# Optimization experiments

Measured on AMD Instinct MI355X. Metric: run time of the kernel, lower is better.

## Reference

```python
import itertools
import jax, jax.numpy as jnp
import numpy as np

# static block configuration
B, C, H, W, DIM, HEADS = 2, 4, 60, 120, 512, 8
WS = (2, 6, 12)          # window size (Wc, Wh, Ww)
SS = (1, 3, 6)           # shift size
N = WS[0] * WS[1] * WS[2]            # 144 tokens per window
C1, H1, W1 = C // WS[0], H // WS[1], W // WS[2]
NW = C1 * H1 * W1                    # windows per sample
DH = DIM // HEADS
EPS = 1e-6


def _attn_bias():
    """Static shifted-window attention bias (nW, N, N): 0 within group, -inf across.
    Mirrors compute_3d_shifted_window_mask (warped=True, longitude wrap merge)."""
    img = np.zeros((C, H, W), np.int32)
    c_sl = ((0, C - WS[0]), (C - WS[0], C - SS[0]), (C - SS[0], C))
    h_sl = ((0, H - WS[1]), (H - WS[1], H - SS[1]), (H - SS[1], H))
    w_sl = ((0, W - WS[2]), (W - WS[2], W - SS[2]), (W - SS[2], W))
    cnt = 0
    for (cs, ce), (hs, he), (ws_, we) in itertools.product(c_sl, h_sl, w_sl):
        img[cs:ce, hs:he, ws_:we] = cnt
        cnt += 1
    # warped (periodic longitude) group merges
    for i in range(3):
        for a, b in ((1, 2), (4, 5), (7, 8)):
            img[img == a + 9 * i] = b + 9 * i
    m = img.reshape(C1, WS[0], H1, WS[1], W1, WS[2])
    m = m.transpose(0, 2, 4, 1, 3, 5).reshape(NW, N)
    diff = m[:, None, :] - m[:, :, None]
    return jnp.asarray(np.where(diff != 0, -np.inf, 0.0).astype(np.float32))


_BIAS = _attn_bias()[None, :, None, :, :]  # (1, nW, 1, N, N)


def _ln(x, s, b):
    mu = x.mean(-1, keepdims=True)
    var = x.var(-1, keepdims=True)
    return (x - mu) / jnp.sqrt(var + EPS) * s + b


def setup_inputs() -> dict:
    key = jax.random.key(0)
    ks = jax.random.split(key, 6)
    s = 0.02
    return {
        "x": jax.random.normal(ks[0], (B, C * H * W, DIM), jnp.float32),
        "qkv_w": jax.random.normal(ks[1], (DIM, 3 * DIM), jnp.float32) * s,
        "qkv_b": jnp.zeros((3 * DIM,), jnp.float32),
        "proj_w": jax.random.normal(ks[2], (DIM, DIM), jnp.float32) * s,
        "proj_b": jnp.zeros((DIM,), jnp.float32),
        "norm1_scale": jnp.ones((DIM,), jnp.float32),
        "norm1_bias": jnp.zeros((DIM,), jnp.float32),
        "norm2_scale": jnp.ones((DIM,), jnp.float32),
        "norm2_bias": jnp.zeros((DIM,), jnp.float32),
        "mlp_w1": jax.random.normal(ks[3], (DIM, 4 * DIM), jnp.float32) * s,
        "mlp_b1": jnp.zeros((4 * DIM,), jnp.float32),
        "mlp_w2": jax.random.normal(ks[4], (4 * DIM, DIM), jnp.float32) * s,
        "mlp_b2": jnp.zeros((DIM,), jnp.float32),
    }


def reference(x, qkv_w, qkv_b, proj_w, proj_b, norm1_scale, norm1_bias,
              norm2_scale, norm2_bias, mlp_w1, mlp_b1, mlp_w2, mlp_b2):
    shortcut = x                                   # (B, L, D)
    h = _ln(x, norm1_scale, norm1_bias).reshape(B, C, H, W, DIM)
    # cyclic shift
    h = jnp.roll(h, (-SS[0], -SS[1], -SS[2]), axis=(1, 2, 3))
    # window partition: (B,C,H,W,D) -> (B*nW, N, D)
    h = h.reshape(B, C1, WS[0], H1, WS[1], W1, WS[2], DIM)
    h = h.transpose(0, 1, 3, 5, 2, 4, 6, 7).reshape(B * NW, N, DIM)
    # windowed multi-head self-attention
    qkv = h @ qkv_w + qkv_b                        # (B*nW, N, 3*D)
    qkv = qkv.reshape(B, NW, N, 3, HEADS, DH)
    q = qkv[..., 0, :, :].transpose(0, 1, 3, 2, 4)  # (B, nW, H, N, Dh)
    k = qkv[..., 1, :, :].transpose(0, 1, 3, 2, 4)
    v = qkv[..., 2, :, :].transpose(0, 1, 3, 2, 4)
    scale = 1.0 / float(np.sqrt(DH))
    attn = jnp.einsum("bwhnd,bwhmd->bwhnm", q, k) * scale + _BIAS
    attn = jax.nn.softmax(attn, axis=-1)
    o = jnp.einsum("bwhnm,bwhmd->bwhnd", attn, v)
    o = o.transpose(0, 1, 3, 2, 4).reshape(B * NW, N, DIM)
    o = o @ proj_w + proj_b
    # window reverse: (B*nW, N, D) -> (B,C,H,W,D)
    o = o.reshape(B, C1, H1, W1, WS[0], WS[1], WS[2], DIM)
    o = o.transpose(0, 1, 4, 2, 5, 3, 6, 7).reshape(B, C, H, W, DIM)
    # reverse cyclic shift
    o = jnp.roll(o, SS, axis=(1, 2, 3))
    x = shortcut + o.reshape(B, C * H * W, DIM)    # drop_path is identity
    # MLP block
    h2 = _ln(x, norm2_scale, norm2_bias)
    h2 = jax.nn.gelu(h2 @ mlp_w1 + mlp_b1) @ mlp_w2 + mlp_b2
    return x + h2
```

## Files before the change

kernel.cpp:

```cpp
#include <hip/hip_runtime.h>

typedef __attribute__((ext_vector_type(8))) short bf16x8;
typedef __attribute__((ext_vector_type(4))) float f32x4;
typedef __attribute__((ext_vector_type(8))) unsigned short u16x8;

#define BAR() __builtin_amdgcn_s_barrier()
#define VMC(n) asm volatile("s_waitcnt vmcnt(" #n ")" ::: "memory")
#define SB0() __builtin_amdgcn_sched_barrier(0)
#define WAITL() do { asm volatile("s_waitcnt lgkmcnt(0)"); SB0(); } while (0)
#define DSRI(dst, base, imm) \
  asm volatile("ds_read_b128 %0, %1 offset:%2" : "=&v"(dst) : "v"(base), "i"(imm))

__device__ inline unsigned short f2bf(float f) {
  unsigned int u = __float_as_uint(f);
  u += 0x7fffu + ((u >> 16) & 1u);
  return (unsigned short)(u >> 16);
}

__device__ inline void gload_lds16(const void* g, void* l) {
  __builtin_amdgcn_global_load_lds(
      (const __attribute__((address_space(1))) void*)g,
      (__attribute__((address_space(3))) void*)l, 16, 0, 0);
}

__global__ void wtrans(const float* __restrict__ W, unsigned short* __restrict__ Wt,
                       int K, int N) {
  int idx = blockIdx.x * 256 + threadIdx.x;
  if (idx >= K * N) return;
  int k = idx / N, n = idx - k * N;
  Wt[(size_t)n * K + k] = f2bf(W[idx]);
}

template <int MODE>
__global__ void ln_k(const float* __restrict__ x, const float* __restrict__ sc,
                     const float* __restrict__ bi, unsigned short* __restrict__ o) {
  int t = blockIdx.x * 4 + (threadIdx.x >> 6);
  int l = threadIdx.x & 63;
  size_t src;
  if (MODE == 0) {
    int b = t / 28800, r = t - b * 28800;
    int win = r / 144, tok = r - win * 144;
    int c1 = win / 100, rem = win - c1 * 100;
    int h1 = rem / 10, w1 = rem - h1 * 10;
    int tc = tok / 72, tr = tok - tc * 72;
    int th = tr / 12, tw = tr - th * 12;
    int cs = c1 * 2 + tc, hs = h1 * 6 + th, wsp = w1 * 12 + tw;
    int co = (cs + 1) & 3;
    int ho = hs + 3; if (ho >= 60) ho -= 60;
    int wo = wsp + 6; if (wo >= 120) wo -= 120;
    src = ((size_t)b * 28800 + (co * 60 + ho) * 120 + wo) * 512;
  } else {
    src = (size_t)t * 512;
  }
  const float4* xr = (const float4*)(x + src);
  float4 v0 = xr[l * 2], v1 = xr[l * 2 + 1];
  float s = v0.x + v0.y + v0.z + v0.w + v1.x + v1.y + v1.z + v1.w;
  float s2 = v0.x * v0.x + v0.y * v0.y + v0.z * v0.z + v0.w * v0.w +
             v1.x * v1.x + v1.y * v1.y + v1.z * v1.z + v1.w * v1.w;
  #pragma unroll
  for (int o2 = 32; o2; o2 >>= 1) {
    s += __shfl_xor(s, o2);
    s2 += __shfl_xor(s2, o2);
  }
  float mean = s * (1.0f / 512.0f);
  float var = s2 * (1.0f / 512.0f) - mean * mean;
  float inv = rsqrtf(var + 1e-6f);
  const float4* scp = (const float4*)sc;
  const float4* bip = (const float4*)bi;
  float4 sa = scp[l * 2], sb = scp[l * 2 + 1];
  float4 ba = bip[l * 2], bb = bip[l * 2 + 1];
  u16x8 ov;
  ov[0] = f2bf((v0.x - mean) * inv * sa.x + ba.x);
  ov[1] = f2bf((v0.y - mean) * inv * sa.y + ba.y);
  ov[2] = f2bf((v0.z - mean) * inv * sa.z + ba.z);
  ov[3] = f2bf((v0.w - mean) * inv * sa.w + ba.w);
  ov[4] = f2bf((v1.x - mean) * inv * sb.x + bb.x);
  ov[5] = f2bf((v1.y - mean) * inv * sb.y + bb.y);
  ov[6] = f2bf((v1.z - mean) * inv * sb.z + bb.z);
  ov[7] = f2bf((v1.w - mean) * inv * sb.w + bb.w);
  *(u16x8*)&o[(size_t)t * 512 + l * 8] = ov;
}

template <int EPI>
__launch_bounds__(256, 2)
__global__ void gemmT(const unsigned short* __restrict__ A,
                      const unsigned short* __restrict__ Bt,
                      const float* __restrict__ bias, void* __restrict__ outp,
                      const float* __restrict__ res, int M, int N, int K) {
  __shared__ __attribute__((aligned(16))) unsigned short lds3[3][12288];
  const int tid = threadIdx.x;
  const int w = tid >> 6, l = tid & 63;
  const int lane15 = l & 15, lk = (l >> 4) << 3;
  const int ntile = N >> 8;
  const int nwg = gridDim.x;
  const int q = nwg >> 3, r = nwg & 7;
  const int xcd = blockIdx.x & 7, idx8 = blockIdx.x >> 3;
  const int wgid = (xcd < r ? xcd * (q + 1) : r * (q + 1) + (xcd - r) * q) + idx8;
  const int bm = wgid / ntile, bn = wgid - bm * ntile;
  const int KT = K >> 5;

  const int swzb = ((l >> 3) & 3) << 3;
  const int colx = (((l & 3) << 3) ^ swzb);
  const int rA0 = (0 * 4 + w) * 16 + (l >> 2);
  const int rA1 = (1 * 4 + w) * 16 + (l >> 2);
  const int offA0 = (rA0 * K + colx) * 2, offA1 = (rA1 * K + colx) * 2;
  int offB[4];
  #pragma unroll
  for (int j = 0; j < 4; ++j)
    offB[j] = (((j * 4 + w) * 16 + (l >> 2)) * K + colx) * 2;

  const int sw = ((lane15 >> 1) & 3) << 3;
  unsigned lds0 = (unsigned)(unsigned long long)
      (__attribute__((address_space(3))) void*)(void*)&lds3[0][0];
  const unsigned comA = (unsigned)(lane15 * 64 + ((lk ^ sw) << 1));
  unsigned bA0 = lds0 + comA;
  unsigned bA1 = bA0 + 24576u, bA2 = bA0 + 49152u;
  const unsigned bOffB = 8192u + ((unsigned)w << 12);
  unsigned bB0 = bA0 + bOffB, bB1 = bA1 + bOffB, bB2 = bA2 + bOffB;

  unsigned short* p0 = &lds3[0][0];
  unsigned short* p1 = &lds3[1][0];
  unsigned short* p2 = &lds3[2][0];

  const char* gA = (const char*)(A + (size_t)bm * 128 * K);
  const char* gB = (const char*)(Bt + (size_t)bn * 256 * K);

  f32x4 acc[8][4] = {};
  bf16x8 afL[4], afH[4], bfr[4];

  auto STAGE = [&](unsigned short* pS, const char* ga, const char* gb) {
    gload_lds16(ga + offA0, pS + w * 512);
    gload_lds16(ga + offA1, pS + 2048 + w * 512);
    #pragma unroll
    for (int j = 0; j < 4; ++j)
      gload_lds16(gb + offB[j], pS + 4096 + (j * 4 + w) * 512);
  };

  STAGE(p0, gA, gB); gA += 64; gB += 64;
  STAGE(p1, gA, gB); gA += 64; gB += 64;
  VMC(6);
  BAR();

  for (int t = 0; t < KT; ++t) {
    DSRI(afL[0], bA0, 0);    DSRI(afL[1], bA0, 1024);
    DSRI(afL[2], bA0, 2048); DSRI(afL[3], bA0, 3072);
    DSRI(bfr[0], bB0, 0);    DSRI(bfr[1], bB0, 1024);
    DSRI(bfr[2], bB0, 2048); DSRI(bfr[3], bB0, 3072);
    if (t < KT - 2) {
      STAGE(p2, gA, gB);
      gA += 64; gB += 64;
    }
    WAITL();
    DSRI(afH[0], bA0, 4096); DSRI(afH[1], bA0, 5120);
    DSRI(afH[2], bA0, 6144); DSRI(afH[3], bA0, 7168);
    SB0();
    __builtin_amdgcn_s_setprio(1);
    #pragma unroll
    for (int mf = 0; mf < 4; ++mf)
      #pragma unroll
      for (int nf = 0; nf < 4; ++nf)
        acc[mf][nf] = __builtin_amdgcn_mfma_f32_16x16x32_bf16(
            afL[mf], bfr[nf], acc[mf][nf], 0, 0, 0);
    __builtin_amdgcn_s_setprio(0);
    WAITL();
    __builtin_amdgcn_s_setprio(1);
    #pragma unroll
    for (int mf = 0; mf < 4; ++mf)
      #pragma unroll
      for (int nf = 0; nf < 4; ++nf)
        acc[4 + mf][nf] = __builtin_amdgcn_mfma_f32_16x16x32_bf16(
            afH[mf], bfr[nf], acc[4 + mf][nf], 0, 0, 0);
    __builtin_amdgcn_s_setprio(0);
    if (t < KT - 2) { VMC(6); } else if (t == KT - 2) { VMC(0); }
    if (t < KT - 1) BAR();
    unsigned ta = bA0; bA0 = bA1; bA1 = bA2; bA2 = ta;
    unsigned tb = bB0; bB0 = bB1; bB1 = bB2; bB2 = tb;
    unsigned short* tp = p0; p0 = p1; p1 = p2; p2 = tp;
  }

  float* outf = (float*)outp;
  unsigned short* outh = (unsigned short*)outp;
  #pragma unroll
  for (int mi = 0; mi < 8; ++mi) {
    #pragma unroll
    for (int j = 0; j < 4; ++j) {
      int grow = bm * 128 + mi * 16 + ((l >> 4) << 2) + j;
      int win = 0, tok = 0;
      size_t rowbase = 0;
      if constexpr (EPI == 0) {
        win = grow / 144;
        tok = grow - win * 144;
      } else if constexpr (EPI == 1) {
        win = grow / 144;
        tok = grow - win * 144;
        int b = win / 200, wl = win - b * 200;
        int c1 = wl / 100, rem = wl - c1 * 100;
        int h1 = rem / 10, w1 = rem - h1 * 10;
        int tc = tok / 72, tr = tok - tc * 72;
        int th = tr / 12, tw = tr - th * 12;
        int cs = c1 * 2 + tc, hs = h1 * 6 + th, wsp = w1 * 12 + tw;
        int co = (cs + 1) & 3;
        int ho = hs + 3; if (ho >= 60) ho -= 60;
        int wo = wsp + 6; if (wo >= 120) wo -= 120;
        rowbase = ((size_t)b * 28800 + (co * 60 + ho) * 120 + wo) * 512;
      }
      #pragma unroll
      for (int nf = 0; nf < 4; ++nf) {
        int gcol = bn * 256 + w * 64 + nf * 16 + lane15;
        float val = acc[mi][nf][j] + bias[gcol];
        if constexpr (EPI == 0) {
          int which = gcol >> 9, hd = (gcol >> 6) & 7, dh = gcol & 63;
          outh[(((size_t)(win * 3 + which) * 8 + hd) * 144 + tok) * 64 + dh] = f2bf(val);
        } else if constexpr (EPI == 1) {
          size_t oi = rowbase + gcol;
          outf[oi] = res[oi] + val;
        } else if constexpr (EPI == 2) {
          float u = 0.7978845608f * (val + 0.044715f * val * val * val);
          float g = val / (1.0f + __expf(-2.0f * u));
          outh[(size_t)grow * N + gcol] = f2bf(g);
        } else {
          size_t oi = (size_t)grow * N + gcol;
          outf[oi] += val;
        }
      }
    }
  }
}

__launch_bounds__(576)
__global__ void attn_k(const unsigned short* __restrict__ qkv,
                       unsigned short* __restrict__ owin) {
  __shared__ __attribute__((aligned(16))) unsigned short Ks[144 * 72];
  __shared__ __attribute__((aligned(16))) unsigned short Vt[64 * 168];
  __shared__ __attribute__((aligned(16))) unsigned short Ps[144 * 168];
  __shared__ unsigned char gid[144];
  int bid = blockIdx.x;
  int win = bid >> 3, head = bid & 7;
  const unsigned short* qb = qkv + ((size_t)(win * 3 + 0) * 8 + head) * (144 * 64);
  const unsigned short* kb = qkv + ((size_t)(win * 3 + 1) * 8 + head) * (144 * 64);
  const unsigned short* vb = qkv + ((size_t)(win * 3 + 2) * 8 + head) * (144 * 64);
  int tid = threadIdx.x;
  {
    int row = tid >> 2, c0 = (tid & 3) << 4;
    u16x8 ka = *(const u16x8*)(kb + row * 64 + c0);
    u16x8 kc = *(const u16x8*)(kb + row * 64 + c0 + 8);
    *(u16x8*)&Ks[row * 72 + c0] = ka;
    *(u16x8*)&Ks[row * 72 + c0 + 8] = kc;
    u16x8 va = *(const u16x8*)(vb + row * 64 + c0);
    u16x8 vc = *(const u16x8*)(vb + row * 64 + c0 + 8);
    #pragma unroll
    for (int j = 0; j < 8; ++j) Vt[(c0 + j) * 168 + row] = va[j];
    #pragma unroll
    for (int j = 0; j < 8; ++j) Vt[(c0 + 8 + j) * 168 + row] = vc[j];
  }
  for (int i = tid; i < 64 * 24; i += 576) {
    int d = i / 24, m = i - d * 24;
    Vt[d * 168 + 144 + m] = 0;
  }
  for (int i = tid; i < 144 * 24; i += 576) {
    int r = i / 24, c = i - r * 24;
    Ps[r * 168 + 144 + c] = 0;
  }
  if (tid < 144) {
    int wl = win % 200;
    int c1 = wl / 100, rem = wl - c1 * 100;
    int h1 = rem / 10, w1 = rem - h1 * 10;
    int tc = tid / 72, tr = tid - tc * 72;
    int th = tr / 12, tw = tr - th * 12;
    int cs = c1 * 2 + tc, hs = h1 * 6 + th, wsp = w1 * 12 + tw;
    int rc = cs < 2 ? 0 : (cs < 3 ? 1 : 2);
    int rh = hs < 54 ? 0 : (hs < 57 ? 1 : 2);
    int rw = wsp < 108 ? 0 : (wsp < 114 ? 1 : 2);
    if (rw == 1) rw = 2;
    gid[tid] = (unsigned char)(rc * 9 + rh * 3 + rw);
  }
  __syncthreads();
  int wv = tid >> 6, l = tid & 63;
  int lane15 = l & 15, lk = (l >> 4) << 3;
  bf16x8 aq0 = *(const bf16x8*)(qb + (wv * 16 + lane15) * 64 + lk);
  bf16x8 aq1 = *(const bf16x8*)(qb + (wv * 16 + lane15) * 64 + 32 + lk);
  f32x4 sf[9];
  #pragma unroll
  for (int ct = 0; ct < 9; ++ct) {
    f32x4 z = {};
    bf16x8 b0 = *(const bf16x8*)&Ks[(ct * 16 + lane15) * 72 + lk];
    bf16x8 b1 = *(const bf16x8*)&Ks[(ct * 16 + lane15) * 72 + 32 + lk];
    z = __builtin_amdgcn_mfma_f32_16x16x32_bf16(aq0, b0, z, 0, 0, 0);
    z = __builtin_amdgcn_mfma_f32_16x16x32_bf16(aq1, b1, z, 0, 0, 0);
    sf[ct] = z;
  }
  int gi[4];
  #pragma unroll
  for (int j = 0; j < 4; ++j) gi[j] = gid[wv * 16 + ((l >> 4) << 2) + j];
  float mx[4] = {-1e30f, -1e30f, -1e30f, -1e30f};
  #pragma unroll
  for (int ct = 0; ct < 9; ++ct) {
    int gj = gid[ct * 16 + lane15];
    #pragma unroll
    for (int j = 0; j < 4; ++j) {
      float s = sf[ct][j] * 0.125f;
      if (gj != gi[j]) s = -1e30f;
      sf[ct][j] = s;
      mx[j] = fmaxf(mx[j], s);
    }
  }
  #pragma unroll
  for (int o2 = 8; o2; o2 >>= 1)
    #pragma unroll
    for (int j = 0; j < 4; ++j) mx[j] = fmaxf(mx[j], __shfl_xor(mx[j], o2));
  float sm[4] = {0.f, 0.f, 0.f, 0.f};
  #pragma unroll
  for (int ct = 0; ct < 9; ++ct)
    #pragma unroll
    for (int j = 0; j < 4; ++j) {
      float e = __expf(sf[ct][j] - mx[j]);
      sf[ct][j] = e;
      sm[j] += e;
    }
  #pragma unroll
  for (int o2 = 8; o2; o2 >>= 1)
    #pragma unroll
    for (int j = 0; j < 4; ++j) sm[j] += __shfl_xor(sm[j], o2);
  float rs[4];
  #pragma unroll
  for (int j = 0; j < 4; ++j) rs[j] = 1.0f / sm[j];
  #pragma unroll
  for (int ct = 0; ct < 9; ++ct)
    #pragma unroll
    for (int j = 0; j < 4; ++j)
      Ps[(wv * 16 + ((l >> 4) << 2) + j) * 168 + ct * 16 + lane15] =
          f2bf(sf[ct][j] * rs[j]);
  __syncthreads();
  f32x4 of[4] = {};
  #pragma unroll
  for (int ks = 0; ks < 5; ++ks) {
    bf16x8 ap = *(const bf16x8*)&Ps[(wv * 16 + lane15) * 168 + ks * 32 + lk];
    #pragma unroll
    for (int nt = 0; nt < 4; ++nt) {
      bf16x8 bv = *(const bf16x8*)&Vt[(nt * 16 + lane15) * 168 + ks * 32 + lk];
      of[nt] = __builtin_amdgcn_mfma_f32_16x16x32_bf16(ap, bv, of[nt], 0, 0, 0);
    }
  }
  unsigned short* ob = owin + (size_t)win * 144 * 512 + head * 64;
  #pragma unroll
  for (int nt = 0; nt < 4; ++nt)
    #pragma unroll
    for (int j = 0; j < 4; ++j) {
      int row = wv * 16 + ((l >> 4) << 2) + j;
      ob[(size_t)row * 512 + nt * 16 + lane15] = f2bf(of[nt][j]);
    }
}

extern "C" void kernel_launch(void* const* d_in, const int* in_sizes, int n_in,
                              void* d_out, int out_size, void* d_ws, size_t ws_size,
                              hipStream_t stream) {
  const float* x = (const float*)d_in[0];
  const float* qkv_w = (const float*)d_in[1];
  const float* qkv_b = (const float*)d_in[2];
  const float* proj_w = (const float*)d_in[3];
  const float* proj_b = (const float*)d_in[4];
  const float* n1s = (const float*)d_in[5];
  const float* n1b = (const float*)d_in[6];
  const float* n2s = (const float*)d_in[7];
  const float* n2b = (const float*)d_in[8];
  const float* w1 = (const float*)d_in[9];
  const float* b1 = (const float*)d_in[10];
  const float* w2 = (const float*)d_in[11];
  const float* b2 = (const float*)d_in[12];
  float* out = (float*)d_out;
  char* ws = (char*)d_ws;

  unsigned short* WqT = (unsigned short*)(ws);
  unsigned short* WpT = (unsigned short*)(ws + 1572864);
  unsigned short* W1T = (unsigned short*)(ws + 2097152);
  unsigned short* W2T = (unsigned short*)(ws + 4194304);
  unsigned short* hwin = (unsigned short*)(ws + 6291456);
  unsigned short* qkvb = (unsigned short*)(ws + 65273856);
  unsigned short* owin = (unsigned short*)(ws + 242221056);
  unsigned short* mid = qkvb;

  wtrans<<<(512 * 1536 + 255) / 256, 256, 0, stream>>>(qkv_w, WqT, 512, 1536);
  wtrans<<<(512 * 512 + 255) / 256, 256, 0, stream>>>(proj_w, WpT, 512, 512);
  wtrans<<<(512 * 2048 + 255) / 256, 256, 0, stream>>>(w1, W1T, 512, 2048);
  wtrans<<<(2048 * 512 + 255) / 256, 256, 0, stream>>>(w2, W2T, 2048, 512);
  ln_k<0><<<14400, 256, 0, stream>>>(x, n1s, n1b, hwin);
  gemmT<0><<<450 * 6, 256, 0, stream>>>(hwin, WqT, qkv_b, qkvb, nullptr, 57600, 1536, 512);
  attn_k<<<3200, 576, 0, stream>>>(qkvb, owin);
  gemmT<1><<<450 * 2, 256, 0, stream>>>(owin, WpT, proj_b, out, x, 57600, 512, 512);
  ln_k<1><<<14400, 256, 0, stream>>>(out, n2s, n2b, hwin);
  gemmT<2><<<450 * 8, 256, 0, stream>>>(hwin, W1T, b1, mid, nullptr, 57600, 2048, 512);
  gemmT<3><<<450 * 2, 256, 0, stream>>>(mid, W2T, b2, out, nullptr, 57600, 512, 2048);
}
```

Baseline: 793.1 us.

## Load GEMM B-operand fragments directly from global into registers, bypassing LDS

The GEMM no longer stages the weight (B) tile through shared memory. Each wave loads its private B fragments straight from global memory into registers, double-buffered across K steps, while A keeps a triple-buffered LDS pipeline. The LDS footprint shrinks to a third, and the two B ds_read batches per K step go away. In exchange every wave issues uncoalesced 16-byte global loads for B, and there is more register pressure from the two B fragment sets and eight A fragments held at once.

```diff
diff --git a/kernel.cpp b/kernel.cpp
--- a/kernel.cpp
+++ b/kernel.cpp
@@ -83,11 +83,11 @@
 
 template <int EPI>
 __launch_bounds__(256, 2)
-__global__ void gemmT(const unsigned short* __restrict__ A,
+__global__ void gemmB(const unsigned short* __restrict__ A,
                       const unsigned short* __restrict__ Bt,
                       const float* __restrict__ bias, void* __restrict__ outp,
                       const float* __restrict__ res, int M, int N, int K) {
-  __shared__ __attribute__((aligned(16))) unsigned short lds3[3][12288];
+  __shared__ __attribute__((aligned(16))) unsigned short ldsA[3][4096];
   const int tid = threadIdx.x;
   const int w = tid >> 6, l = tid & 63;
   const int lane15 = l & 15, lk = (l >> 4) << 3;
@@ -101,81 +101,82 @@
 
   const int swzb = ((l >> 3) & 3) << 3;
   const int colx = (((l & 3) << 3) ^ swzb);
-  const int rA0 = (0 * 4 + w) * 16 + (l >> 2);
-  const int rA1 = (1 * 4 + w) * 16 + (l >> 2);
-  const int offA0 = (rA0 * K + colx) * 2, offA1 = (rA1 * K + colx) * 2;
-  int offB[4];
-  #pragma unroll
-  for (int j = 0; j < 4; ++j)
-    offB[j] = (((j * 4 + w) * 16 + (l >> 2)) * K + colx) * 2;
+  const int offA0 = ((w * 16 + (l >> 2)) * K + colx) * 2;
+  const int offA1 = (((4 + w) * 16 + (l >> 2)) * K + colx) * 2;
 
   const int sw = ((lane15 >> 1) & 3) << 3;
   unsigned lds0 = (unsigned)(unsigned long long)
-      (__attribute__((address_space(3))) void*)(void*)&lds3[0][0];
-  const unsigned comA = (unsigned)(lane15 * 64 + ((lk ^ sw) << 1));
-  unsigned bA0 = lds0 + comA;
-  unsigned bA1 = bA0 + 24576u, bA2 = bA0 + 49152u;
-  const unsigned bOffB = 8192u + ((unsigned)w << 12);
-  unsigned bB0 = bA0 + bOffB, bB1 = bA1 + bOffB, bB2 = bA2 + bOffB;
-
-  unsigned short* p0 = &lds3[0][0];
-  unsigned short* p1 = &lds3[1][0];
-  unsigned short* p2 = &lds3[2][0];
+      (__attribute__((address_space(3))) void*)(void*)&ldsA[0][0];
+  unsigned bA0 = lds0 + (unsigned)(lane15 * 64 + ((lk ^ sw) << 1));
+  unsigned bA1 = bA0 + 8192u, bA2 = bA0 + 16384u;
+  unsigned short* p0 = &ldsA[0][0];
+  unsigned short* p1 = &ldsA[1][0];
+  unsigned short* p2 = &ldsA[2][0];
 
   const char* gA = (const char*)(A + (size_t)bm * 128 * K);
-  const char* gB = (const char*)(Bt + (size_t)bn * 256 * K);
+
+  const unsigned short* gBf[4];
+  #pragma unroll
+  for (int nf = 0; nf < 4; ++nf)
+    gBf[nf] = Bt + (size_t)(bn * 256 + w * 64 + nf * 16 + lane15) * K + lk;
 
   f32x4 acc[8][4] = {};
-  bf16x8 afL[4], afH[4], bfr[4];
-
-  auto STAGE = [&](unsigned short* pS, const char* ga, const char* gb) {
+  bf16x8 af[8], bP[4], bN[4];
+
+  auto STAGEA = [&](unsigned short* pS, const char* ga) {
     gload_lds16(ga + offA0, pS + w * 512);
     gload_lds16(ga + offA1, pS + 2048 + w * 512);
-    #pragma unroll
-    for (int j = 0; j < 4; ++j)
-      gload_lds16(gb + offB[j], pS + 4096 + (j * 4 + w) * 512);
   };
-
-  STAGE(p0, gA, gB); gA += 64; gB += 64;
-  STAGE(p1, gA, gB); gA += 64; gB += 64;
-  VMC(6);
-  BAR();
-
-  for (int t = 0; t < KT; ++t) {
-    DSRI(afL[0], bA0, 0);    DSRI(afL[1], bA0, 1024);
-    DSRI(afL[2], bA0, 2048); DSRI(afL[3], bA0, 3072);
-    DSRI(bfr[0], bB0, 0);    DSRI(bfr[1], bB0, 1024);
-    DSRI(bfr[2], bB0, 2048); DSRI(bfr[3], bB0, 3072);
-    if (t < KT - 2) {
-      STAGE(p2, gA, gB);
-      gA += 64; gB += 64;
-    }
-    WAITL();
-    DSRI(afH[0], bA0, 4096); DSRI(afH[1], bA0, 5120);
-    DSRI(afH[2], bA0, 6144); DSRI(afH[3], bA0, 7168);
-    SB0();
+  auto MFMA32 = [&](bf16x8* bu) {
     __builtin_amdgcn_s_setprio(1);
     #pragma unroll
-    for (int mf = 0; mf < 4; ++mf)
+    for (int mi = 0; mi < 8; ++mi)
       #pragma unroll
       for (int nf = 0; nf < 4; ++nf)
-        acc[mf][nf] = __builtin_amdgcn_mfma_f32_16x16x32_bf16(
-            afL[mf], bfr[nf], acc[mf][nf], 0, 0, 0);
+        acc[mi][nf] = __builtin_amdgcn_mfma_f32_16x16x32_bf16(
+            af[mi], bu[nf], acc[mi][nf], 0, 0, 0);
     __builtin_amdgcn_s_setprio(0);
+  };
+
+  STAGEA(p0, gA);
+  STAGEA(p1, gA + 64);
+  gA += 128;
+  #pragma unroll
+  for (int nf = 0; nf < 4; ++nf) { bP[nf] = *(const bf16x8*)gBf[nf]; gBf[nf] += 32; }
+  VMC(0);
+  BAR();
+
+  for (int t = 0; t < KT; t += 2) {
+    DSRI(af[0], bA0, 0);    DSRI(af[1], bA0, 1024);
+    DSRI(af[2], bA0, 2048); DSRI(af[3], bA0, 3072);
+    DSRI(af[4], bA0, 4096); DSRI(af[5], bA0, 5120);
+    DSRI(af[6], bA0, 6144); DSRI(af[7], bA0, 7168);
+    if (t + 2 < KT) { STAGEA(p2, gA); gA += 64; }
+    if (t + 1 < KT) {
+      #pragma unroll
+      for (int nf = 0; nf < 4; ++nf) { bN[nf] = *(const bf16x8*)gBf[nf]; gBf[nf] += 32; }
+    }
+    if (t + 2 < KT) { VMC(6); } else if (t + 1 < KT) { VMC(4); } else { VMC(0); }
     WAITL();
-    __builtin_amdgcn_s_setprio(1);
-    #pragma unroll
-    for (int mf = 0; mf < 4; ++mf)
+    MFMA32(bP);
+    BAR();
+    { unsigned ta = bA0; bA0 = bA1; bA1 = bA2; bA2 = ta;
+      unsigned short* tp = p0; p0 = p1; p1 = p2; p2 = tp; }
+    DSRI(af[0], bA0, 0);    DSRI(af[1], bA0, 1024);
+    DSRI(af[2], bA0, 2048); DSRI(af[3], bA0, 3072);
+    DSRI(af[4], bA0, 4096); DSRI(af[5], bA0, 5120);
+    DSRI(af[6], bA0, 6144); DSRI(af[7], bA0, 7168);
+    if (t + 3 < KT) { STAGEA(p2, gA); gA += 64; }
+    if (t + 2 < KT) {
       #pragma unroll
-      for (int nf = 0; nf < 4; ++nf)
-        acc[4 + mf][nf] = __builtin_amdgcn_mfma_f32_16x16x32_bf16(
-            afH[mf], bfr[nf], acc[4 + mf][nf], 0, 0, 0);
-    __builtin_amdgcn_s_setprio(0);
-    if (t < KT - 2) { VMC(6); } else if (t == KT - 2) { VMC(0); }
-    if (t < KT - 1) BAR();
-    unsigned ta = bA0; bA0 = bA1; bA1 = bA2; bA2 = ta;
-    unsigned tb = bB0; bB0 = bB1; bB1 = bB2; bB2 = tb;
-    unsigned short* tp = p0; p0 = p1; p1 = p2; p2 = tp;
+      for (int nf = 0; nf < 4; ++nf) { bP[nf] = *(const bf16x8*)gBf[nf]; gBf[nf] += 32; }
+    }
+    if (t + 3 < KT) { VMC(6); } else if (t + 2 < KT) { VMC(4); } else { VMC(0); }
+    WAITL();
+    MFMA32(bN);
+    BAR();
+    { unsigned ta = bA0; bA0 = bA1; bA1 = bA2; bA2 = ta;
+      unsigned short* tp = p0; p0 = p1; p1 = p2; p2 = tp; }
   }
 
   float* outf = (float*)outp;
@@ -384,10 +385,10 @@
   wtrans<<<(512 * 2048 + 255) / 256, 256, 0, stream>>>(w1, W1T, 512, 2048);
   wtrans<<<(2048 * 512 + 255) / 256, 256, 0, stream>>>(w2, W2T, 2048, 512);
   ln_k<0><<<14400, 256, 0, stream>>>(x, n1s, n1b, hwin);
-  gemmT<0><<<450 * 6, 256, 0, stream>>>(hwin, WqT, qkv_b, qkvb, nullptr, 57600, 1536, 512);
+  gemmB<0><<<450 * 6, 256, 0, stream>>>(hwin, WqT, qkv_b, qkvb, nullptr, 57600, 1536, 512);
   attn_k<<<3200, 576, 0, stream>>>(qkvb, owin);
-  gemmT<1><<<450 * 2, 256, 0, stream>>>(owin, WpT, proj_b, out, x, 57600, 512, 512);
+  gemmB<1><<<450 * 2, 256, 0, stream>>>(owin, WpT, proj_b, out, x, 57600, 512, 512);
   ln_k<1><<<14400, 256, 0, stream>>>(out, n2s, n2b, hwin);
-  gemmT<2><<<450 * 8, 256, 0, stream>>>(hwin, W1T, b1, mid, nullptr, 57600, 2048, 512);
-  gemmT<3><<<450 * 2, 256, 0, stream>>>(mid, W2T, b2, out, nullptr, 57600, 512, 2048);
-}
+  gemmB<2><<<450 * 8, 256, 0, stream>>>(hwin, W1T, b1, mid, nullptr, 57600, 2048, 512);
+  gemmB<3><<<450 * 2, 256, 0, stream>>>(mid, W2T, b2, out, nullptr, 57600, 512, 2048);
+}
```

After: 898.2 us. 1.13x slower.
